# Kernel optimization log

Measured on AMD Instinct MI355X. Metric: run time of the kernel, lower is better.

The kernel has to match this reference:

```python
import jax, jax.numpy as jnp
import numpy as np

DIM = 64  # per-head dim; temperature init = sqrt(DIM)
B, H, S, D = 4, 12, 2048, 64


def setup_inputs() -> dict:
    key = jax.random.key(0)
    kq, kk, kv = jax.random.split(key, 3)
    Q = jax.random.normal(kq, (B, H, S, D), dtype=jnp.float32)
    K = jax.random.normal(kk, (B, H, S, D), dtype=jnp.float32)
    V = jax.random.normal(kv, (B, H, S, D), dtype=jnp.float32)
    temperature = jnp.ones((1,), dtype=jnp.float32) * (DIM ** 0.5)
    return {"Q": Q, "K": K, "V": V, "temperature": temperature}


def reference(Q, K, V, temperature):
    # scores: [B,H,S,S]
    scores = jnp.einsum("bhqd,bhkd->bhqk", Q, K) / temperature
    s = scores.shape[-1]
    eye = jnp.eye(s, dtype=bool)  # diagonal self-exclusion
    scores = jnp.where(eye, -jnp.inf, scores)
    attn = jax.nn.softmax(scores, axis=-1)
    return jnp.einsum("bhqk,bhkd->bhqd", attn, V)
```

## Files before the change

### kernel.cpp

```cpp
#include <hip/hip_runtime.h>
#include <hip/hip_bf16.h>

#define S_LEN 2048
#define D_DIM 64
#define NHEADS 48
#define QT 128
#define KT 64
#define NKT (S_LEN / KT)
#define HEAD_ELEMS ((size_t)S_LEN * D_DIM)
#define WS_NEED (3ull * NHEADS * S_LEN * D_DIM * 2ull)

typedef short bf16x8 __attribute__((ext_vector_type(8)));
typedef float f32x4 __attribute__((ext_vector_type(4)));

__device__ __forceinline__ unsigned short f2bf(float x) {
    unsigned u = __builtin_bit_cast(unsigned, x);
    u = (u + 0x7fffu + ((u >> 16) & 1u)) >> 16;
    return (unsigned short)u;
}

__device__ __forceinline__ unsigned cvtpk(float lo, float hi) {
    unsigned r;
    asm("v_cvt_pk_bf16_f32 %0, %1, %2" : "=v"(r) : "v"(lo), "v"(hi));
    return r;
}

__device__ __forceinline__ void gload16(const void* g, void* l) {
    __builtin_amdgcn_global_load_lds(
        (const __attribute__((address_space(1))) unsigned int*)g,
        (__attribute__((address_space(3))) unsigned int*)l, 16, 0, 0);
}

__global__ __launch_bounds__(256) void lsa_prep(
    const float* __restrict__ Qg, const float* __restrict__ Kg,
    const float* __restrict__ Vg, const float* __restrict__ Tg,
    unsigned short* __restrict__ Qs, unsigned short* __restrict__ Kf,
    unsigned short* __restrict__ Vf) {
    const int b   = blockIdx.x;
    const int tid = threadIdx.x;
    const int r   = tid >> 4;
    const int c4  = (tid & 15) * 4;

    __shared__ __align__(16) unsigned short Kl[4096];
    __shared__ __align__(16) unsigned short Vl[4096];

    const size_t ibase = (size_t)b * 4096;
    const float qscale = 1.442695041f / Tg[0];

#pragma unroll
    for (int it = 0; it < 4; ++it) {
        const int rr = it * 16 + r;
        const size_t off = ibase + (size_t)rr * D_DIM + c4;

        float4 q4 = *(const float4*)(Qg + off);
        uint2 qo;
        qo.x = cvtpk(q4.x * qscale, q4.y * qscale);
        qo.y = cvtpk(q4.z * qscale, q4.w * qscale);
        *(uint2*)&Qs[off] = qo;

        float4 k4 = *(const float4*)(Kg + off);
        {
            const int f = rr >> 4, l15 = rr & 15;
            const int c = c4 >> 5, lhi = (c4 >> 3) & 3, j0 = c4 & 7;
            uint2 ko;
            ko.x = cvtpk(k4.x, k4.y);
            ko.y = cvtpk(k4.z, k4.w);
            *(uint2*)&Kl[c * 2048 + f * 512 + ((lhi << 4) | l15) * 8 + j0] = ko;
        }

        float4 v4 = *(const float4*)(Vg + off);
        {
            const int cc = rr >> 5, rem = rr & 31;
            const int jv = ((rem >> 4) << 2) | (rem & 3);
            const int lhiv = (rem >> 2) & 3;
            const int g = c4 >> 4;
            const int base = cc * 2048 + g * 512 + (lhiv << 7) + jv;
            Vl[base + ((c4 + 0) & 15) * 8] = f2bf(v4.x);
            Vl[base + ((c4 + 1) & 15) * 8] = f2bf(v4.y);
            Vl[base + ((c4 + 2) & 15) * 8] = f2bf(v4.z);
            Vl[base + ((c4 + 3) & 15) * 8] = f2bf(v4.w);
        }
    }
    __syncthreads();
    const uint4* ks = (const uint4*)Kl;
    const uint4* vs = (const uint4*)Vl;
    uint4* kd = (uint4*)(Kf + ibase);
    uint4* vd = (uint4*)(Vf + ibase);
    kd[tid]       = ks[tid];
    kd[tid + 256] = ks[tid + 256];
    vd[tid]       = vs[tid];
    vd[tid + 256] = vs[tid + 256];
}

__global__ __launch_bounds__(256, 2) void lsa_attn_ns2(
    const unsigned short* __restrict__ Qs, const unsigned short* __restrict__ Kf,
    const unsigned short* __restrict__ Vf, float* __restrict__ Og) {

    const int bid  = blockIdx.x;
    const int xcd  = bid & 7;
    const int idx  = bid >> 3;
    const int bh   = xcd * 6 + (idx >> 4);
    const int qt   = idx & 15;
    const int tid  = threadIdx.x;
    const int wid  = tid >> 6;
    const int lane = tid & 63;
    const int l15  = lane & 15;
    const int lhi  = lane >> 4;

    __shared__ __align__(16) unsigned short KV[2][2][KT * D_DIM];

    const unsigned short* Qh = Qs + (size_t)bh * HEAD_ELEMS;
    const char* Kh = (const char*)(Kf + (size_t)bh * HEAD_ELEMS);
    const char* Vh = (const char*)(Vf + (size_t)bh * HEAD_ELEMS);
    float* Ob = Og + (size_t)bh * HEAD_ELEMS;

    const int qbase   = qt * QT + wid * 32;
    const int diag_kt = qbase >> 6;

    bf16x8 qf[2][2];
#pragma unroll
    for (int rb = 0; rb < 2; ++rb) {
#pragma unroll
        for (int c = 0; c < 2; ++c) {
            qf[rb][c] = *(const bf16x8*)(Qh + (size_t)(qbase + rb * 16 + l15) * D_DIM
                                            + c * 32 + lhi * 8);
        }
    }

    const f32x4 zero4 = {0.f, 0.f, 0.f, 0.f};
    f32x4 acc[2][4];
    f32x4 lp4[2];
#pragma unroll
    for (int rb = 0; rb < 2; ++rb) {
#pragma unroll
        for (int g = 0; g < 4; ++g) acc[rb][g] = zero4;
        lp4[rb] = zero4;
    }

    bf16x8 vr[8];
    f32x4 sf[2][4];
    bf16x8 pb[2][2];

#define ISSUE(BUF, T) do {                                                     \
    const char* ks_ = Kh + (size_t)(T) * 8192 + wid * 2048;                    \
    const char* vs_ = Vh + (size_t)(T) * 8192 + wid * 2048;                    \
    char* lk_ = (char*)&KV[BUF][0][0] + wid * 2048;                            \
    char* lv_ = (char*)&KV[BUF][1][0] + wid * 2048;                            \
    gload16(ks_ + lane * 16, lk_);                                             \
    gload16(ks_ + 1024 + lane * 16, lk_ + 1024);                               \
    gload16(vs_ + lane * 16, lv_);                                             \
    gload16(vs_ + 1024 + lane * 16, lv_ + 1024);                               \
} while (0)

#define DSQK(BUF) do {                                                         \
    const char* lk_ = (const char*)&KV[BUF][0][0] + lane * 16;                 \
    _Pragma("unroll")                                                          \
    for (int rb = 0; rb < 2; ++rb) {                                           \
        _Pragma("unroll")                                                      \
        for (int f = 0; f < 4; ++f) sf[rb][f] = zero4;                         \
    }                                                                          \
    _Pragma("unroll")                                                          \
    for (int c = 0; c < 2; ++c) {                                              \
        bf16x8 kb_[4];                                                         \
        _Pragma("unroll")                                                      \
        for (int f = 0; f < 4; ++f) {                                          \
            kb_[f] = *(const bf16x8*)(lk_ + c * 4096 + f * 1024);              \
        }                                                                      \
        __builtin_amdgcn_s_setprio(1);                                         \
        _Pragma("unroll")                                                      \
        for (int rb = 0; rb < 2; ++rb) {                                       \
            _Pragma("unroll")                                                  \
            for (int f = 0; f < 4; ++f) {                                      \
                sf[rb][f] = __builtin_amdgcn_mfma_f32_16x16x32_bf16(           \
                    kb_[f], qf[rb][c], sf[rb][f], 0, 0, 0);                    \
            }                                                                  \
        }                                                                      \
        __builtin_amdgcn_s_setprio(0);                                         \
    }                                                                          \
} while (0)

#define DSV(BUF) do {                                                          \
    const char* lv_ = (const char*)&KV[BUF][1][0] + lane * 16;                 \
    _Pragma("unroll")                                                          \
    for (int u = 0; u < 8; ++u) {                                              \
        vr[u] = *(const bf16x8*)(lv_ + (u >> 2) * 4096 + (u & 3) * 1024);      \
    }                                                                          \
} while (0)

#define PV() do {                                                              \
    __builtin_amdgcn_s_setprio(1);                                             \
    _Pragma("unroll")                                                          \
    for (int cc = 0; cc < 2; ++cc) {                                           \
        _Pragma("unroll")                                                      \
        for (int rb = 0; rb < 2; ++rb) {                                       \
            _Pragma("unroll")                                                  \
            for (int g = 0; g < 4; ++g) {                                      \
                acc[rb][g] = __builtin_amdgcn_mfma_f32_16x16x32_bf16(          \
                    vr[cc * 4 + g], pb[rb][cc], acc[rb][g], 0, 0, 0);          \
            }                                                                  \
        }                                                                      \
    }                                                                          \
    __builtin_amdgcn_s_setprio(0);                                             \
} while (0)

#define SMX(T) do {                                                            \
    if ((T) == diag_kt) {                                                      \
        _Pragma("unroll")                                                      \
        for (int rb = 0; rb < 2; ++rb) {                                       \
            const int q_ = qbase + rb * 16 + l15;                              \
            _Pragma("unroll")                                                  \
            for (int f = 0; f < 4; ++f) {                                      \
                _Pragma("unroll")                                              \
                for (int i = 0; i < 4; ++i) {                                  \
                    const int k_ = (T) * KT + f * 16 + lhi * 4 + i;            \
                    if (q_ == k_) sf[rb][f][i] = -1e30f;                       \
                }                                                              \
            }                                                                  \
        }                                                                      \
    }                                                                          \
    _Pragma("unroll")                                                          \
    for (int rb = 0; rb < 2; ++rb) {                                           \
        _Pragma("unroll")                                                      \
        for (int f = 0; f < 4; ++f) {                                          \
            _Pragma("unroll")                                                  \
            for (int i = 0; i < 4; ++i) {                                      \
                sf[rb][f][i] = __builtin_amdgcn_exp2f(sf[rb][f][i]);           \
            }                                                                  \
            lp4[rb] += sf[rb][f];                                              \
        }                                                                      \
        _Pragma("unroll")                                                      \
        for (int cc = 0; cc < 2; ++cc) {                                       \
            uint4 u_;                                                          \
            u_.x = cvtpk(sf[rb][cc * 2][0],     sf[rb][cc * 2][1]);            \
            u_.y = cvtpk(sf[rb][cc * 2][2],     sf[rb][cc * 2][3]);            \
            u_.z = cvtpk(sf[rb][cc * 2 + 1][0], sf[rb][cc * 2 + 1][1]);        \
            u_.w = cvtpk(sf[rb][cc * 2 + 1][2], sf[rb][cc * 2 + 1][3]);        \
            pb[rb][cc] = __builtin_bit_cast(bf16x8, u_);                       \
        }                                                                      \
    }                                                                          \
} while (0)

    ISSUE(0, 0);
    __syncthreads();
    ISSUE(1, 1);
    DSQK(0);
    DSV(0);

#pragma unroll 1
    for (int t = 0; t < NKT - 1; ++t) {
        SMX(t);
        PV();
        __syncthreads();
        if (t + 2 < NKT) ISSUE(t & 1, t + 2);
        DSQK((t + 1) & 1);
        DSV((t + 1) & 1);
    }
    SMX(NKT - 1);
    PV();

#undef ISSUE
#undef DSQK
#undef DSV
#undef PV
#undef SMX

#pragma unroll
    for (int rb = 0; rb < 2; ++rb) {
        float l = (lp4[rb][0] + lp4[rb][1]) + (lp4[rb][2] + lp4[rb][3]);
        l += __shfl_xor(l, 16);
        l += __shfl_xor(l, 32);
        const float invl = 1.0f / l;
        const int q = qbase + rb * 16 + l15;
#pragma unroll
        for (int g = 0; g < 4; ++g) {
            float4 o;
            o.x = acc[rb][g][0] * invl;
            o.y = acc[rb][g][1] * invl;
            o.z = acc[rb][g][2] * invl;
            o.w = acc[rb][g][3] * invl;
            *(float4*)(Ob + (size_t)q * D_DIM + g * 16 + lhi * 4) = o;
        }
    }
}

__device__ __forceinline__ int swzK_fb(int row, int col) {
    return (row << 6) + (col ^ ((row & 7) << 3));
}
__device__ __forceinline__ int swzV_fb(int row, int col) {
    int f = (row ^ (row >> 3)) & 7;
    return (row << 6) + (col ^ (f << 3));
}

__global__ __launch_bounds__(256, 2) void lsa_attn_fb(
    const float* __restrict__ Qg, const float* __restrict__ Kg,
    const float* __restrict__ Vg, const float* __restrict__ Tg,
    float* __restrict__ Og) {

    const int bid  = blockIdx.x;
    const int bh   = bid >> 4;
    const int qt   = bid & 15;
    const int tid  = threadIdx.x;
    const int wid  = tid >> 6;
    const int lane = tid & 63;
    const int l15  = lane & 15;
    const int lhi  = lane >> 4;

    __shared__ __align__(16) unsigned short Kt[64 * D_DIM];
    __shared__ __align__(16) unsigned short Vt[D_DIM * 64];

    const size_t base = (size_t)bh * HEAD_ELEMS;
    const float* Qb = Qg + base;
    const float* Kb = Kg + base;
    const float* Vb = Vg + base;
    float*       Ob = Og + base;

    const float inv_t = 1.0f / Tg[0];
    const int qbase = qt * QT + wid * 32;
    const int diag_kt = qbase >> 6;

    bf16x8 qf[2][2];
#pragma unroll
    for (int rb = 0; rb < 2; ++rb) {
#pragma unroll
        for (int c = 0; c < 2; ++c) {
            const float* src = Qb + (size_t)(qbase + rb * 16 + l15) * D_DIM + c * 32 + lhi * 8;
            float4 a = *(const float4*)(src);
            float4 b = *(const float4*)(src + 4);
            bf16x8 v;
            v[0] = (short)f2bf(a.x * inv_t); v[1] = (short)f2bf(a.y * inv_t);
            v[2] = (short)f2bf(a.z * inv_t); v[3] = (short)f2bf(a.w * inv_t);
            v[4] = (short)f2bf(b.x * inv_t); v[5] = (short)f2bf(b.y * inv_t);
            v[6] = (short)f2bf(b.z * inv_t); v[7] = (short)f2bf(b.w * inv_t);
            qf[rb][c] = v;
        }
    }

    const f32x4 zero4 = {0.f, 0.f, 0.f, 0.f};
    f32x4 acc[2][4];
    float mrow[2], lrow[2];
#pragma unroll
    for (int rb = 0; rb < 2; ++rb) {
#pragma unroll
        for (int g = 0; g < 4; ++g) acc[rb][g] = zero4;
        mrow[rb] = -1e30f; lrow[rb] = 0.f;
    }

    const int ld_r = tid >> 4;
    const int ld_c = (tid & 15) * 4;
    float4 kreg[4], vreg[4];

#define LOAD_TILE(KT_IDX) do {                                                 \
    const int kb0_ = (KT_IDX) * 64;                                            \
    _Pragma("unroll")                                                          \
    for (int it = 0; it < 4; ++it) {                                           \
        const int r_ = it * 16 + ld_r;                                         \
        kreg[it] = *(const float4*)(Kb + (size_t)(kb0_ + r_) * D_DIM + ld_c);  \
        vreg[it] = *(const float4*)(Vb + (size_t)(kb0_ + r_) * D_DIM + ld_c);  \
    }                                                                          \
} while (0)

    LOAD_TILE(0);

    for (int kt = 0; kt < 32; ++kt) {
        const int kb0 = kt * 64;
        __syncthreads();
#pragma unroll
        for (int it = 0; it < 4; ++it) {
            const int r = it * 16 + ld_r;
            unsigned lo = (unsigned)f2bf(kreg[it].x) | ((unsigned)f2bf(kreg[it].y) << 16);
            unsigned hi = (unsigned)f2bf(kreg[it].z) | ((unsigned)f2bf(kreg[it].w) << 16);
            *(uint2*)&Kt[swzK_fb(r, ld_c)] = make_uint2(lo, hi);
            Vt[swzV_fb(ld_c + 0, r)] = f2bf(vreg[it].x);
            Vt[swzV_fb(ld_c + 1, r)] = f2bf(vreg[it].y);
            Vt[swzV_fb(ld_c + 2, r)] = f2bf(vreg[it].z);
            Vt[swzV_fb(ld_c + 3, r)] = f2bf(vreg[it].w);
        }
        __syncthreads();
        if (kt + 1 < 32) LOAD_TILE(kt + 1);

        f32x4 sf[2][4];
#pragma unroll
        for (int rb = 0; rb < 2; ++rb) {
#pragma unroll
            for (int f = 0; f < 4; ++f) sf[rb][f] = zero4;
        }

#pragma unroll
        for (int c = 0; c < 2; ++c) {
            bf16x8 kb[4];
#pragma unroll
            for (int f = 0; f < 4; ++f)
                kb[f] = *(const bf16x8*)&Kt[swzK_fb(f * 16 + l15, c * 32 + lhi * 8)];
#pragma unroll
            for (int rb = 0; rb < 2; ++rb) {
#pragma unroll
                for (int f = 0; f < 4; ++f)
                    sf[rb][f] = __builtin_amdgcn_mfma_f32_16x16x32_bf16(
                        kb[f], qf[rb][c], sf[rb][f], 0, 0, 0);
            }
        }

        if (kt == diag_kt) {
#pragma unroll
            for (int rb = 0; rb < 2; ++rb) {
                const int q = qbase + rb * 16 + l15;
#pragma unroll
                for (int f = 0; f < 4; ++f) {
#pragma unroll
                    for (int i = 0; i < 4; ++i) {
                        const int k = kb0 + f * 16 + lhi * 4 + i;
                        if (q == k) sf[rb][f][i] = -1e30f;
                    }
                }
            }
        }

        bf16x8 pb[2][2];
#pragma unroll
        for (int rb = 0; rb < 2; ++rb) {
            f32x4 mv;
#pragma unroll
            for (int i = 0; i < 4; ++i)
                mv[i] = fmaxf(fmaxf(sf[rb][0][i], sf[rb][1][i]),
                              fmaxf(sf[rb][2][i], sf[rb][3][i]));
            float m0 = fmaxf(fmaxf(mv[0], mv[1]), fmaxf(mv[2], mv[3]));
            m0 = fmaxf(m0, __shfl_xor(m0, 16));
            m0 = fmaxf(m0, __shfl_xor(m0, 32));
            const float mnew  = fmaxf(mrow[rb], m0);
            const float alpha = __expf(mrow[rb] - mnew);
            mrow[rb] = mnew;
            f32x4 ps = zero4;
#pragma unroll
            for (int f = 0; f < 4; ++f) {
#pragma unroll
                for (int i = 0; i < 4; ++i)
                    sf[rb][f][i] = __expf(sf[rb][f][i] - mnew);
                ps += sf[rb][f];
            }
            float s0 = (ps[0] + ps[1]) + (ps[2] + ps[3]);
            s0 += __shfl_xor(s0, 16);
            s0 += __shfl_xor(s0, 32);
            lrow[rb] = lrow[rb] * alpha + s0;
#pragma unroll
            for (int g = 0; g < 4; ++g) acc[rb][g] *= alpha;
#pragma unroll
            for (int cc = 0; cc < 2; ++cc) {
                bf16x8 v;
#pragma unroll
                for (int j = 0; j < 8; ++j)
                    v[j] = (short)f2bf(sf[rb][cc * 2 + (j >> 2)][j & 3]);
                pb[rb][cc] = v;
            }
        }

#pragma unroll
        for (int cc = 0; cc < 2; ++cc) {
            bf16x8 va[4];
#pragma unroll
            for (int g = 0; g < 4; ++g) {
                const int row = g * 16 + l15;
                uint2 lo = *(const uint2*)&Vt[swzV_fb(row, cc * 32 + lhi * 4)];
                uint2 hi = *(const uint2*)&Vt[swzV_fb(row, cc * 32 + 16 + lhi * 4)];
                bf16x8 t;
                ((uint2*)&t)[0] = lo;
                ((uint2*)&t)[1] = hi;
                va[g] = t;
            }
#pragma unroll
            for (int rb = 0; rb < 2; ++rb) {
#pragma unroll
                for (int g = 0; g < 4; ++g)
                    acc[rb][g] = __builtin_amdgcn_mfma_f32_16x16x32_bf16(
                        va[g], pb[rb][cc], acc[rb][g], 0, 0, 0);
            }
        }
    }
#undef LOAD_TILE

#pragma unroll
    for (int rb = 0; rb < 2; ++rb) {
        const float invl = 1.0f / lrow[rb];
        const int q = qbase + rb * 16 + l15;
#pragma unroll
        for (int g = 0; g < 4; ++g) {
            float4 o;
            o.x = acc[rb][g][0] * invl;
            o.y = acc[rb][g][1] * invl;
            o.z = acc[rb][g][2] * invl;
            o.w = acc[rb][g][3] * invl;
            *(float4*)(Ob + (size_t)q * D_DIM + g * 16 + lhi * 4) = o;
        }
    }
}

extern "C" void kernel_launch(void* const* d_in, const int* in_sizes, int n_in,
                              void* d_out, int out_size, void* d_ws, size_t ws_size,
                              hipStream_t stream) {
    const float* Q = (const float*)d_in[0];
    const float* K = (const float*)d_in[1];
    const float* V = (const float*)d_in[2];
    const float* T = (const float*)d_in[3];
    float* O = (float*)d_out;

    if (ws_size >= WS_NEED) {
        unsigned short* Qs = (unsigned short*)d_ws;
        unsigned short* Kf = Qs + NHEADS * HEAD_ELEMS;
        unsigned short* Vf = Kf + NHEADS * HEAD_ELEMS;
        hipLaunchKernelGGL(lsa_prep, dim3(NHEADS * NKT), dim3(256), 0, stream,
                           Q, K, V, T, Qs, Kf, Vf);
        hipLaunchKernelGGL(lsa_attn_ns2, dim3(NHEADS * (S_LEN / QT)), dim3(256), 0, stream,
                           Qs, Kf, Vf, O);
    } else {
        hipLaunchKernelGGL(lsa_attn_fb, dim3(NHEADS * (S_LEN / QT)), dim3(256), 0, stream,
                           Q, K, V, T, O);
    }
}
```

Baseline: 75.16 us.

## Switch attention MFMAs from 16x16x32 to 32x32x16 tiles with matching K/V layout

```diff
diff --git a/kernel.cpp b/kernel.cpp
--- a/kernel.cpp
+++ b/kernel.cpp
@@ -12,6 +12,7 @@
 
 typedef short bf16x8 __attribute__((ext_vector_type(8)));
 typedef float f32x4 __attribute__((ext_vector_type(4)));
+typedef float f32x16 __attribute__((ext_vector_type(16)));
 
 __device__ __forceinline__ unsigned short f2bf(float x) {
     unsigned u = __builtin_bit_cast(unsigned, x);
@@ -60,25 +61,28 @@
 
         float4 k4 = *(const float4*)(Kg + off);
         {
-            const int f = rr >> 4, l15 = rr & 15;
-            const int c = c4 >> 5, lhi = (c4 >> 3) & 3, j0 = c4 & 7;
+            const int fK = rr >> 5, row32 = rr & 31;
+            const int sK = c4 >> 4, dd = c4 & 15;
+            const int hiK = dd >> 3, j0 = dd & 7;
             uint2 ko;
             ko.x = cvtpk(k4.x, k4.y);
             ko.y = cvtpk(k4.z, k4.w);
-            *(uint2*)&Kl[c * 2048 + f * 512 + ((lhi << 4) | l15) * 8 + j0] = ko;
+            *(uint2*)&Kl[fK * 2048 + sK * 512 + ((hiK << 5) | row32) * 8 + j0] = ko;
         }
 
         float4 v4 = *(const float4*)(Vg + off);
         {
-            const int cc = rr >> 5, rem = rr & 31;
-            const int jv = ((rem >> 4) << 2) | (rem & 3);
-            const int lhiv = (rem >> 2) & 3;
-            const int g = c4 >> 4;
-            const int base = cc * 2048 + g * 512 + (lhiv << 7) + jv;
-            Vl[base + ((c4 + 0) & 15) * 8] = f2bf(v4.x);
-            Vl[base + ((c4 + 1) & 15) * 8] = f2bf(v4.y);
-            Vl[base + ((c4 + 2) & 15) * 8] = f2bf(v4.z);
-            Vl[base + ((c4 + 3) & 15) * 8] = f2bf(v4.w);
+            const int fV  = rr >> 5, rem = rr & 31;
+            const int hiV = (rem >> 2) & 1;
+            const int rrr = (rem & 3) + 4 * (rem >> 3);
+            const int idxV = fV * 16 + rrr;
+            const int sV = idxV >> 3, jV = idxV & 7;
+            const int gV = c4 >> 5, colb = c4 & 31;
+            const int vb = gV * 2048 + sV * 512 + (hiV << 5) * 8 + jV;
+            Vl[vb + (colb + 0) * 8] = f2bf(v4.x);
+            Vl[vb + (colb + 1) * 8] = f2bf(v4.y);
+            Vl[vb + (colb + 2) * 8] = f2bf(v4.z);
+            Vl[vb + (colb + 3) * 8] = f2bf(v4.w);
         }
     }
     __syncthreads();
@@ -92,7 +96,7 @@
     vd[tid + 256] = vs[tid + 256];
 }
 
-__global__ __launch_bounds__(256, 2) void lsa_attn_ns2(
+__global__ __launch_bounds__(256, 2) void lsa_attn_w32(
     const unsigned short* __restrict__ Qs, const unsigned short* __restrict__ Kf,
     const unsigned short* __restrict__ Vf, float* __restrict__ Og) {
 
@@ -104,8 +108,8 @@
     const int tid  = threadIdx.x;
     const int wid  = tid >> 6;
     const int lane = tid & 63;
-    const int l15  = lane & 15;
-    const int lhi  = lane >> 4;
+    const int l31  = lane & 31;
+    const int hi   = lane >> 5;
 
     __shared__ __align__(16) unsigned short KV[2][2][KT * D_DIM];
 
@@ -116,30 +120,24 @@
 
     const int qbase   = qt * QT + wid * 32;
     const int diag_kt = qbase >> 6;
-
-    bf16x8 qf[2][2];
-#pragma unroll
-    for (int rb = 0; rb < 2; ++rb) {
-#pragma unroll
-        for (int c = 0; c < 2; ++c) {
-            qf[rb][c] = *(const bf16x8*)(Qh + (size_t)(qbase + rb * 16 + l15) * D_DIM
-                                            + c * 32 + lhi * 8);
-        }
-    }
-
+    const int qrow    = qbase + l31;
+
+    bf16x8 qf[4];
+#pragma unroll
+    for (int s = 0; s < 4; ++s) {
+        qf[s] = *(const bf16x8*)(Qh + (size_t)qrow * D_DIM + s * 16 + hi * 8);
+    }
+
+    const f32x16 zero16 = {0.f,0.f,0.f,0.f,0.f,0.f,0.f,0.f,
+                           0.f,0.f,0.f,0.f,0.f,0.f,0.f,0.f};
     const f32x4 zero4 = {0.f, 0.f, 0.f, 0.f};
-    f32x4 acc[2][4];
-    f32x4 lp4[2];
-#pragma unroll
-    for (int rb = 0; rb < 2; ++rb) {
-#pragma unroll
-        for (int g = 0; g < 4; ++g) acc[rb][g] = zero4;
-        lp4[rb] = zero4;
-    }
+    f32x16 acc[2];
+    f32x4  lp4;
+    acc[0] = zero16; acc[1] = zero16; lp4 = zero4;
 
     bf16x8 vr[8];
-    f32x4 sf[2][4];
-    bf16x8 pb[2][2];
+    f32x16 sf[2];
+    bf16x8 pb[4];
 
 #define ISSUE(BUF, T) do {                                                     \
     const char* ks_ = Kh + (size_t)(T) * 8192 + wid * 2048;                    \
@@ -154,26 +152,19 @@
 
 #define DSQK(BUF) do {                                                         \
     const char* lk_ = (const char*)&KV[BUF][0][0] + lane * 16;                 \
+    sf[0] = zero16; sf[1] = zero16;                                            \
     _Pragma("unroll")                                                          \
-    for (int rb = 0; rb < 2; ++rb) {                                           \
-        _Pragma("unroll")                                                      \
-        for (int f = 0; f < 4; ++f) sf[rb][f] = zero4;                         \
-    }                                                                          \
-    _Pragma("unroll")                                                          \
-    for (int c = 0; c < 2; ++c) {                                              \
+    for (int f = 0; f < 2; ++f) {                                              \
         bf16x8 kb_[4];                                                         \
         _Pragma("unroll")                                                      \
-        for (int f = 0; f < 4; ++f) {                                          \
-            kb_[f] = *(const bf16x8*)(lk_ + c * 4096 + f * 1024);              \
+        for (int s = 0; s < 4; ++s) {                                          \
+            kb_[s] = *(const bf16x8*)(lk_ + f * 4096 + s * 1024);              \
         }                                                                      \
         __builtin_amdgcn_s_setprio(1);                                         \
         _Pragma("unroll")                                                      \
-        for (int rb = 0; rb < 2; ++rb) {                                       \
-            _Pragma("unroll")                                                  \
-            for (int f = 0; f < 4; ++f) {                                      \
-                sf[rb][f] = __builtin_amdgcn_mfma_f32_16x16x32_bf16(           \
-                    kb_[f], qf[rb][c], sf[rb][f], 0, 0, 0);                    \
-            }                                                                  \
+        for (int s = 0; s < 4; ++s) {                                          \
+            sf[f] = __builtin_amdgcn_mfma_f32_32x32x16_bf16(                   \
+                kb_[s], qf[s], sf[f], 0, 0, 0);                                \
         }                                                                      \
         __builtin_amdgcn_s_setprio(0);                                         \
     }                                                                          \
@@ -190,14 +181,11 @@
 #define PV() do {                                                              \
     __builtin_amdgcn_s_setprio(1);                                             \
     _Pragma("unroll")                                                          \
-    for (int cc = 0; cc < 2; ++cc) {                                           \
+    for (int g = 0; g < 2; ++g) {                                              \
         _Pragma("unroll")                                                      \
-        for (int rb = 0; rb < 2; ++rb) {                                       \
-            _Pragma("unroll")                                                  \
-            for (int g = 0; g < 4; ++g) {                                      \
-                acc[rb][g] = __builtin_amdgcn_mfma_f32_16x16x32_bf16(          \
-                    vr[cc * 4 + g], pb[rb][cc], acc[rb][g], 0, 0, 0);          \
-            }                                                                  \
+        for (int s = 0; s < 4; ++s) {                                          \
+            acc[g] = __builtin_amdgcn_mfma_f32_32x32x16_bf16(                  \
+                vr[g * 4 + s], pb[s], acc[g], 0, 0, 0);                        \
         }                                                                      \
     }                                                                          \
     __builtin_amdgcn_s_setprio(0);                                             \
@@ -206,37 +194,35 @@
 #define SMX(T) do {                                                            \
     if ((T) == diag_kt) {                                                      \
         _Pragma("unroll")                                                      \
-        for (int rb = 0; rb < 2; ++rb) {                                       \
-            const int q_ = qbase + rb * 16 + l15;                              \
+        for (int f = 0; f < 2; ++f) {                                          \
             _Pragma("unroll")                                                  \
-            for (int f = 0; f < 4; ++f) {                                      \
-                _Pragma("unroll")                                              \
-                for (int i = 0; i < 4; ++i) {                                  \
-                    const int k_ = (T) * KT + f * 16 + lhi * 4 + i;            \
-                    if (q_ == k_) sf[rb][f][i] = -1e30f;                       \
-                }                                                              \
+            for (int rr = 0; rr < 16; ++rr) {                                  \
+                const int k_ = (T) * KT + f * 32 + (rr & 3) + 8 * (rr >> 2)    \
+                               + 4 * hi;                                       \
+                if (qrow == k_) sf[f][rr] = -1e30f;                            \
             }                                                                  \
         }                                                                      \
     }                                                                          \
     _Pragma("unroll")                                                          \
-    for (int rb = 0; rb < 2; ++rb) {                                           \
+    for (int f = 0; f < 2; ++f) {                                              \
         _Pragma("unroll")                                                      \
-        for (int f = 0; f < 4; ++f) {                                          \
-            _Pragma("unroll")                                                  \
-            for (int i = 0; i < 4; ++i) {                                      \
-                sf[rb][f][i] = __builtin_amdgcn_exp2f(sf[rb][f][i]);           \
-            }                                                                  \
-            lp4[rb] += sf[rb][f];                                              \
+        for (int rr = 0; rr < 16; ++rr) {                                      \
+            sf[f][rr] = __builtin_amdgcn_exp2f(sf[f][rr]);                     \
         }                                                                      \
         _Pragma("unroll")                                                      \
-        for (int cc = 0; cc < 2; ++cc) {                                       \
-            uint4 u_;                                                          \
-            u_.x = cvtpk(sf[rb][cc * 2][0],     sf[rb][cc * 2][1]);            \
-            u_.y = cvtpk(sf[rb][cc * 2][2],     sf[rb][cc * 2][3]);            \
-            u_.z = cvtpk(sf[rb][cc * 2 + 1][0], sf[rb][cc * 2 + 1][1]);        \
-            u_.w = cvtpk(sf[rb][cc * 2 + 1][2], sf[rb][cc * 2 + 1][3]);        \
-            pb[rb][cc] = __builtin_bit_cast(bf16x8, u_);                       \
+        for (int j = 0; j < 4; ++j) {                                          \
+            lp4[j] += (sf[f][j] + sf[f][4 + j]) + (sf[f][8 + j] + sf[f][12 + j]); \
         }                                                                      \
+    }                                                                          \
+    _Pragma("unroll")                                                          \
+    for (int s = 0; s < 4; ++s) {                                              \
+        const int f_ = s >> 1, rb_ = (s & 1) * 8;                              \
+        uint4 u_;                                                              \
+        u_.x = cvtpk(sf[f_][rb_ + 0], sf[f_][rb_ + 1]);                        \
+        u_.y = cvtpk(sf[f_][rb_ + 2], sf[f_][rb_ + 3]);                        \
+        u_.z = cvtpk(sf[f_][rb_ + 4], sf[f_][rb_ + 5]);                        \
+        u_.w = cvtpk(sf[f_][rb_ + 6], sf[f_][rb_ + 7]);                        \
+        pb[s] = __builtin_bit_cast(bf16x8, u_);                                \
     }                                                                          \
 } while (0)
 
@@ -264,21 +250,21 @@
 #undef PV
 #undef SMX
 
-#pragma unroll
-    for (int rb = 0; rb < 2; ++rb) {
-        float l = (lp4[rb][0] + lp4[rb][1]) + (lp4[rb][2] + lp4[rb][3]);
-        l += __shfl_xor(l, 16);
+    {
+        float l = (lp4[0] + lp4[1]) + (lp4[2] + lp4[3]);
         l += __shfl_xor(l, 32);
         const float invl = 1.0f / l;
-        const int q = qbase + rb * 16 + l15;
-#pragma unroll
-        for (int g = 0; g < 4; ++g) {
-            float4 o;
-            o.x = acc[rb][g][0] * invl;
-            o.y = acc[rb][g][1] * invl;
-            o.z = acc[rb][g][2] * invl;
-            o.w = acc[rb][g][3] * invl;
-            *(float4*)(Ob + (size_t)q * D_DIM + g * 16 + lhi * 4) = o;
+#pragma unroll
+        for (int g = 0; g < 2; ++g) {
+#pragma unroll
+            for (int rq = 0; rq < 4; ++rq) {
+                float4 o;
+                o.x = acc[g][rq * 4 + 0] * invl;
+                o.y = acc[g][rq * 4 + 1] * invl;
+                o.z = acc[g][rq * 4 + 2] * invl;
+                o.w = acc[g][rq * 4 + 3] * invl;
+                *(float4*)(Ob + (size_t)qrow * D_DIM + g * 32 + rq * 8 + hi * 4) = o;
+            }
         }
     }
 }
@@ -508,7 +494,7 @@
         unsigned short* Vf = Kf + NHEADS * HEAD_ELEMS;
         hipLaunchKernelGGL(lsa_prep, dim3(NHEADS * NKT), dim3(256), 0, stream,
                            Q, K, V, T, Qs, Kf, Vf);
-        hipLaunchKernelGGL(lsa_attn_ns2, dim3(NHEADS * (S_LEN / QT)), dim3(256), 0, stream,
+        hipLaunchKernelGGL(lsa_attn_w32, dim3(NHEADS * (S_LEN / QT)), dim3(256), 0, stream,
                            Qs, Kf, Vf, O);
     } else {
         hipLaunchKernelGGL(lsa_attn_fb, dim3(NHEADS * (S_LEN / QT)), dim3(256), 0, stream,
```

Result: slower. 79.52 us (+5.8%).
